# Optimization experiments

Measured on AMD Instinct MI355X. Metric: run time of the kernel, lower is better.

The kernel has to match this reference:

```python
import jax, jax.numpy as jnp
from jax import lax
import numpy as np

COST_CLASS, COST_BOX, COST_GIOU = 1.0, 5.0, 2.0
B, Q, C, T = 16, 900, 92, 100
INF = jnp.float32(1e18)


def setup_inputs() -> dict:
    key = jax.random.key(0)
    k1, k2, k3, k4 = jax.random.split(key, 4)
    pred_logits = jax.random.normal(k1, (B, Q, C), jnp.float32)

    def mk_boxes(k, n):
        kc, ks = jax.random.split(k)
        cxcy = jax.random.uniform(kc, (B, n, 2), jnp.float32) * 0.8 + 0.1
        wh = jax.random.uniform(ks, (B, n, 2), jnp.float32) * 0.2 + 0.05
        return jnp.concatenate([cxcy, wh], axis=-1)  # valid cxcywh in (0,1)

    pred_boxes = mk_boxes(k2, Q)
    tgt_boxes = mk_boxes(k3, T)
    tgt_labels = jax.random.randint(k4, (B, T), 0, C)
    return {"pred_logits": pred_logits, "pred_boxes": pred_boxes,
            "tgt_labels": tgt_labels, "tgt_boxes": tgt_boxes}


def box_cxcywh_to_xyxy(b):
    cx, cy, w, h = b[..., 0], b[..., 1], b[..., 2], b[..., 3]
    return jnp.stack([cx - 0.5 * w, cy - 0.5 * h, cx + 0.5 * w, cy + 0.5 * h], axis=-1)


def generalized_box_iou(a, b):
    # a: [B,Q,4] xyxy, b: [B,T,4] xyxy -> [B,Q,T]
    area_a = (a[..., 2] - a[..., 0]) * (a[..., 3] - a[..., 1])  # [B,Q]
    area_b = (b[..., 2] - b[..., 0]) * (b[..., 3] - b[..., 1])  # [B,T]
    a_ = a[:, :, None, :]
    b_ = b[:, None, :, :]
    lt = jnp.maximum(a_[..., :2], b_[..., :2])
    rb = jnp.minimum(a_[..., 2:], b_[..., 2:])
    wh = jnp.clip(rb - lt, 0.0)
    inter = wh[..., 0] * wh[..., 1]
    union = area_a[:, :, None] + area_b[:, None, :] - inter
    iou = inter / union
    lt_c = jnp.minimum(a_[..., :2], b_[..., :2])
    rb_c = jnp.maximum(a_[..., 2:], b_[..., 2:])
    wh_c = jnp.clip(rb_c - lt_c, 0.0)
    area_c = wh_c[..., 0] * wh_c[..., 1]
    return iou - (area_c - union) / area_c


def cost_matrix(pred_logits, pred_boxes, tgt_labels, tgt_boxes):
    probs = jax.nn.softmax(pred_logits, axis=-1)                         # [B,Q,C]
    cost_class = -jnp.take_along_axis(probs, tgt_labels[:, None, :], 2)  # [B,Q,T]
    cost_box = jnp.abs(pred_boxes[:, :, None, :] - tgt_boxes[:, None, :, :]).sum(-1)
    cost_giou = -generalized_box_iou(box_cxcywh_to_xyxy(pred_boxes),
                                     box_cxcywh_to_xyxy(tgt_boxes))
    return COST_BOX * cost_box + COST_CLASS * cost_class + COST_GIOU * cost_giou


def hungarian(cost):
    # Jonker-Volgenant shortest augmenting path. cost: [n, m], n <= m, minimize.
    # Returns col_for_row [n]: column assigned to each row.
    n, m = cost.shape

    def solve_row(i, uvp):
        u, v, p = uvp  # u:[n+1] row potentials, v:[m+1] col potentials, p:[m+1] col->row (n = free)
        p = p.at[m].set(i)  # virtual start column holds current row
        minv = jnp.full((m,), INF, jnp.float32)
        way = jnp.zeros((m,), jnp.int32)
        used = jnp.zeros((m + 1,), bool)
        j0 = jnp.int32(m)

        def cond(s):
            _, _, _, _, _, j0 = s
            return p[j0] != n  # stop when a free column is reached

        def body(s):
            u, v, minv, way, used, j0 = s
            used = used.at[j0].set(True)
            i0 = p[j0]
            cur = cost[i0] - u[i0] - v[:m]           # reduced costs of row i0
            mask = (~used[:m]) & (cur < minv)
            minv = jnp.where(mask, cur, minv)
            way = jnp.where(mask, j0, way)
            mvals = jnp.where(used[:m], INF, minv)
            j1 = jnp.argmin(mvals).astype(jnp.int32)
            delta = mvals[j1]
            u = u.at[p].add(jnp.where(used, delta, 0.0))
            v = v - jnp.where(used, delta, 0.0)
            minv = jnp.where(used[:m], minv, minv - delta)
            return (u, v, minv, way, used, j1)

        u, v, minv, way, used, j0 = lax.while_loop(cond, body, (u, v, minv, way, used, j0))

        def acond(s):
            _, j0 = s
            return j0 != m

        def abody(s):
            p, j0 = s
            j1 = way[j0]
            p = p.at[j0].set(p[j1])
            return (p, j1)

        p, _ = lax.while_loop(acond, abody, (p, j0))
        return (u, v, p)

    u0 = jnp.zeros((n + 1,), jnp.float32)
    v0 = jnp.zeros((m + 1,), jnp.float32)
    p0 = jnp.full((m + 1,), n, jnp.int32)
    _, _, p = lax.fori_loop(0, n, solve_row, (u0, v0, p0))
    col_for_row = jnp.zeros((n + 1,), jnp.int32).at[p[:m]].set(
        jnp.arange(m, dtype=jnp.int32))[:n]
    return col_for_row


def reference(pred_logits, pred_boxes, tgt_labels, tgt_boxes):
    cost = cost_matrix(pred_logits, pred_boxes, tgt_labels, tgt_boxes)  # [B,Q,T]
    # assign each target (row) to a distinct query (col); vmap over batch
    q_per_t = jax.vmap(hungarian)(jnp.swapaxes(cost, 1, 2))  # [B,T]
    order = jnp.argsort(q_per_t, axis=-1)                    # sort by query idx (scipy convention)
    q_idx = jnp.take_along_axis(q_per_t, order, axis=-1)     # query indices  [B,T]
    t_idx = order.astype(jnp.int32)                          # target indices [B,T]
    return cost, q_idx, t_idx
```

## Files before the change

kernel.cpp:

```cpp
#include <hip/hip_runtime.h>

#define BB 16
#define QQ 900
#define QP 960
#define VIRT QP
#define CC 92
#define TT 100
#define INFF 1e18f
#define NK 15

#define DPP_STEP_F(x, ctrl, OP)                                             \
  do {                                                                      \
    float _o = __int_as_float(__builtin_amdgcn_update_dpp(                  \
        __float_as_int(x), __float_as_int(x), (ctrl), 0xF, 0xF, false));    \
    (x) = OP((x), _o);                                                      \
  } while (0)

__device__ __forceinline__ float wave_fmax63(float x) {
  DPP_STEP_F(x, 0xB1, fmaxf);
  DPP_STEP_F(x, 0x4E, fmaxf);
  DPP_STEP_F(x, 0x141, fmaxf);
  DPP_STEP_F(x, 0x140, fmaxf);
  DPP_STEP_F(x, 0x142, fmaxf);
  DPP_STEP_F(x, 0x143, fmaxf);
  return x;
}
__device__ __forceinline__ float wave_fmin63(float x) {
  DPP_STEP_F(x, 0xB1, fminf);
  DPP_STEP_F(x, 0x4E, fminf);
  DPP_STEP_F(x, 0x141, fminf);
  DPP_STEP_F(x, 0x140, fminf);
  DPP_STEP_F(x, 0x142, fminf);
  DPP_STEP_F(x, 0x143, fminf);
  return x;
}
__device__ __forceinline__ float wave_fadd63(float x) {
#define ADDF(a, b) ((a) + (b))
  DPP_STEP_F(x, 0xB1, ADDF);
  DPP_STEP_F(x, 0x4E, ADDF);
  DPP_STEP_F(x, 0x141, ADDF);
  DPP_STEP_F(x, 0x140, ADDF);
  DPP_STEP_F(x, 0x142, ADDF);
  DPP_STEP_F(x, 0x143, ADDF);
#undef ADDF
  return x;
}
__device__ __forceinline__ int wave_imin63(int x) {
  {int _o=__builtin_amdgcn_update_dpp(x,x,0xB1,0xF,0xF,false); x=_o<x?_o:x;}
  {int _o=__builtin_amdgcn_update_dpp(x,x,0x4E,0xF,0xF,false); x=_o<x?_o:x;}
  {int _o=__builtin_amdgcn_update_dpp(x,x,0x141,0xF,0xF,false);x=_o<x?_o:x;}
  {int _o=__builtin_amdgcn_update_dpp(x,x,0x140,0xF,0xF,false);x=_o<x?_o:x;}
  {int _o=__builtin_amdgcn_update_dpp(x,x,0x142,0xF,0xF,false);x=_o<x?_o:x;}
  {int _o=__builtin_amdgcn_update_dpp(x,x,0x143,0xF,0xF,false);x=_o<x?_o:x;}
  return x;
}

#define KEY_STEP(CTRL)                                                      \
  do {                                                                      \
    unsigned olo = (unsigned)__builtin_amdgcn_update_dpp(                   \
        (int)klo, (int)klo, (CTRL), 0xF, 0xF, false);                       \
    unsigned ohi = (unsigned)__builtin_amdgcn_update_dpp(                   \
        (int)khi, (int)khi, (CTRL), 0xF, 0xF, false);                       \
    const unsigned long long cur8 =                                         \
        ((unsigned long long)khi << 32) | klo;                              \
    const unsigned long long oth8 =                                         \
        ((unsigned long long)ohi << 32) | olo;                              \
    if (oth8 < cur8) { khi = ohi; klo = olo; }                              \
  } while (0)

__device__ __forceinline__ void stage_row(const float* __restrict__ row,
                                          float* buf, int lane) {
  typedef __attribute__((address_space(1))) const void gv_t;
  typedef __attribute__((address_space(3))) void lv_t;
  __builtin_amdgcn_global_load_lds((gv_t*)(row + lane * 4),       (lv_t*)(buf),       16, 0, 0);
  __builtin_amdgcn_global_load_lds((gv_t*)(row + 256 + lane * 4), (lv_t*)(buf + 256), 16, 0, 0);
  __builtin_amdgcn_global_load_lds((gv_t*)(row + 512 + lane * 4), (lv_t*)(buf + 512), 16, 0, 0);
  __builtin_amdgcn_global_load_lds((gv_t*)(row + 768 + lane),     (lv_t*)(buf + 768), 4, 0, 0);
  __builtin_amdgcn_global_load_lds((gv_t*)(row + 832 + lane),     (lv_t*)(buf + 832), 4, 0, 0);
  __builtin_amdgcn_global_load_lds((gv_t*)(row + 896 + lane),     (lv_t*)(buf + 896), 4, 0, 0);
}

__device__ __forceinline__ int p_get(unsigned a, unsigned b, unsigned c,
                                     unsigned d, int j) {
  const int l = j & 63, kq = j >> 6;
  unsigned r0 = (unsigned)__builtin_amdgcn_readlane((int)a, l);
  unsigned r1 = (unsigned)__builtin_amdgcn_readlane((int)b, l);
  unsigned r2 = (unsigned)__builtin_amdgcn_readlane((int)c, l);
  unsigned r3 = (unsigned)__builtin_amdgcn_readlane((int)d, l);
  unsigned r = (kq < 8) ? (kq < 4 ? r0 : r1) : (kq < 12 ? r2 : r3);
  return (int)((r >> ((kq & 3) * 8)) & 0xFFu);
}

#define P_SET(jj, val)                                                      \
  do {                                                                      \
    const int _j = (jj); const int _kq = _j >> 6;                           \
    const unsigned _sh = (unsigned)((_kq & 3) * 8);                         \
    const unsigned _nm = ~(0xFFu << _sh);                                   \
    const unsigned _in = ((unsigned)(val) & 0xFFu) << _sh;                  \
    const bool _own = (lane == (_j & 63));                                  \
    if (_kq < 4)       { if (_own) p4a = (p4a & _nm) | _in; }               \
    else if (_kq < 8)  { if (_own) p4b = (p4b & _nm) | _in; }               \
    else if (_kq < 12) { if (_own) p4c = (p4c & _nm) | _in; }               \
    else               { if (_own) p4d = (p4d & _nm) | _in; }               \
  } while (0)

__global__ __launch_bounds__(64) void cost_kernel(
    const float* __restrict__ logits,
    const float* __restrict__ pboxes,
    const int*   __restrict__ tlabels,
    const float* __restrict__ tboxes,
    float* __restrict__ cost,
    float* __restrict__ costT,
    int ctp)
{
  const int bq   = blockIdx.x;
  const int b    = bq / QQ;
  const int q    = bq - b * QQ;
  const int lane = threadIdx.x;

  __shared__ float sl[CC];

  const float a = logits[(size_t)bq * CC + lane];
  const float bb2 = (lane < CC - 64)
                        ? logits[(size_t)bq * CC + 64 + lane]
                        : -3.402823466e38f;

  float mx = fmaxf(a, bb2);
  mx = wave_fmax63(mx);
  const float m = __int_as_float(
      __builtin_amdgcn_readlane(__float_as_int(mx), 63));

  const float e0 = expf(a - m);
  const float e1 = (lane < CC - 64) ? expf(bb2 - m) : 0.0f;
  sl[lane] = e0;
  if (lane < CC - 64) sl[64 + lane] = e1;

  float sm = e0 + e1;
  sm = wave_fadd63(sm);
  const float ssum = __int_as_float(
      __builtin_amdgcn_readlane(__float_as_int(sm), 63));

  const float4 pbv = ((const float4*)pboxes)[bq];
  const float pax1 = pbv.x - 0.5f * pbv.z, pay1 = pbv.y - 0.5f * pbv.w;
  const float pax2 = pbv.x + 0.5f * pbv.z, pay2 = pbv.y + 0.5f * pbv.w;
  const float area_a = (pax2 - pax1) * (pay2 - pay1);

  for (int t = lane; t < TT; t += 64) {
    const int lab = tlabels[b * TT + t];
    const float cc = -(sl[lab] / ssum);

    const float4 tb = ((const float4*)tboxes)[b * TT + t];
    const float cbox = fabsf(pbv.x - tb.x) + fabsf(pbv.y - tb.y) +
                       fabsf(pbv.z - tb.z) + fabsf(pbv.w - tb.w);

    const float bx1 = tb.x - 0.5f * tb.z, by1 = tb.y - 0.5f * tb.w;
    const float bx2 = tb.x + 0.5f * tb.z, by2 = tb.y + 0.5f * tb.w;
    const float area_b = (bx2 - bx1) * (by2 - by1);

    const float ltx = fmaxf(pax1, bx1), lty = fmaxf(pay1, by1);
    const float rbx = fminf(pax2, bx2), rby = fminf(pay2, by2);
    const float iw = fmaxf(rbx - ltx, 0.0f), ih = fmaxf(rby - lty, 0.0f);
    const float inter = iw * ih;
    const float uni = area_a + area_b - inter;
    const float iou = inter / uni;

    const float cx1 = fminf(pax1, bx1), cy1 = fminf(pay1, by1);
    const float cx2 = fmaxf(pax2, bx2), cy2 = fmaxf(pay2, by2);
    const float cw = fmaxf(cx2 - cx1, 0.0f), ch = fmaxf(cy2 - cy1, 0.0f);
    const float ac = cw * ch;
    const float giou = iou - (ac - uni) / ac;

    const float cval = 5.0f * cbox + cc - 2.0f * giou;
    cost[(size_t)bq * TT + t] = cval;
    if (ctp) costT[((size_t)b * TT + t) * ctp + q] = cval;
  }
  if (ctp == QP && q < QP - QQ) {
    for (int t = lane; t < TT; t += 64)
      costT[((size_t)b * TT + t) * QP + QQ + q] = INFF;
  }
}

__global__ void __launch_bounds__(64)
hungarianT_kernel(
    const float* __restrict__ ct,
    float* __restrict__ out_q,
    float* __restrict__ out_t)
{
  const int b    = blockIdx.x;
  const int lane = threadIdx.x;

  __shared__ __align__(16) float rowbuf[2][QP];
  __shared__ int way_lds[QP];
  __shared__ int qpt[TT];

  const float* __restrict__ base = ct + (size_t)b * TT * QP;

  unsigned p4a = 0x64646464u, p4b = 0x64646464u;
  unsigned p4c = 0x64646464u, p4d = 0x64646464u;

  float u0 = 0.0f, u1 = 0.0f;
  float v[NK];
#pragma unroll
  for (int k = 0; k < NK; ++k) v[k] = 0.0f;

  stage_row(base, &rowbuf[0][0], lane);

  for (int i = 0; i < TT; ++i) {
    float* bufc = &rowbuf[i & 1][0];
    float* bufn = &rowbuf[(i + 1) & 1][0];

    float minv[NK];
#pragma unroll
    for (int k = 0; k < NK; ++k) minv[k] = INFF;
    unsigned umask = 0;

    int i0 = i;
    int j0 = VIRT;
    int jfin;

    float us = (i0 < 64) ? u0 : u1;
    float ui0 = __int_as_float(
        __builtin_amdgcn_readlane(__float_as_int(us), i0 & 63));

    for (int step = 0; step < 128; ++step) {
      if (i0 == lane)      umask |= (1u << 30);
      if (i0 == 64 + lane) umask |= (1u << 31);
      if (j0 != VIRT && (j0 & 63) == lane) umask |= (1u << (j0 >> 6));

      asm volatile("s_waitcnt vmcnt(0)" ::: "memory");

      float lmin  = INFF;
      int   kbest = 0;
#pragma unroll
      for (int k = 0; k < NK; ++k) {
        const float ck  = bufc[k * 64 + lane];
        const bool  uk  = (umask >> k) & 1u;
        const float cur = ck - ui0 - v[k];
        const bool  imp = !uk && (cur < minv[k]);
        if (imp) { minv[k] = cur; way_lds[k * 64 + lane] = j0; }
        const float eff = uk ? INFF : minv[k];
        if (eff < lmin) { lmin = eff; kbest = k; }
      }
      const int lidx = (kbest << 6) + lane;

      if (j0 == VIRT && i + 1 < TT)
        stage_row(base + (size_t)(i + 1) * QP, bufn, lane);

      unsigned fb = __float_as_uint(lmin);
      fb = (fb & 0x80000000u) ? ~fb : (fb | 0x80000000u);
      unsigned khi = fb, klo = (unsigned)lidx;
      KEY_STEP(0xB1);
      KEY_STEP(0x4E);
      KEY_STEP(0x141);
      KEY_STEP(0x140);
      KEY_STEP(0x142);
      KEY_STEP(0x143);
      const int j1 = __builtin_amdgcn_readlane((int)klo, 63);
      const unsigned hb =
          (unsigned)__builtin_amdgcn_readlane((int)khi, 63);
      const float delta =
          __uint_as_float((hb & 0x80000000u) ? (hb ^ 0x80000000u) : ~hb);

      const int  i0n = p_get(p4a, p4b, p4c, p4d, j1);
      const bool fin = (i0n == TT);

      if (!fin) stage_row(base + (size_t)i0n * QP, bufc, lane);

      u0 += ((umask >> 30) & 1u) ? delta : 0.0f;
      u1 += (umask >> 31)        ? delta : 0.0f;
#pragma unroll
      for (int k = 0; k < NK; ++k)
        v[k] -= ((umask >> k) & 1u) ? delta : 0.0f;
      if (!fin) {
#pragma unroll
        for (int k = 0; k < NK; ++k)
          minv[k] -= ((umask >> k) & 1u) ? 0.0f : delta;
      }

      if (fin) { jfin = j1; break; }
      float us2 = (i0n < 64) ? u0 : u1;
      ui0 = __int_as_float(
          __builtin_amdgcn_readlane(__float_as_int(us2), i0n & 63));
      j0 = j1;
      i0 = i0n;
    }

    if (j0 == VIRT) {
      P_SET(jfin, i);
    } else {
      int j = jfin;
      for (int hop = 0; hop < 128 && j != VIRT; ++hop) {
        int jn = way_lds[j];
        jn = __builtin_amdgcn_readfirstlane(jn);
        const int pj = (jn == VIRT) ? i : p_get(p4a, p4b, p4c, p4d, jn);
        P_SET(j, pj);
        j = jn;
      }
    }
  }

#pragma unroll
  for (int k = 0; k < NK; ++k) {
    const unsigned reg = (k < 4) ? p4a : (k < 8) ? p4b : (k < 12) ? p4c : p4d;
    const int r = (int)((reg >> ((k & 3) * 8)) & 0xFFu);
    const int j = k * 64 + lane;
    if (r < TT) qpt[r] = j;
  }
  __syncthreads();

  for (int t = lane; t < TT; t += 64) {
    const int myq = qpt[t];
    int rank = 0;
    for (int t2 = 0; t2 < TT; ++t2) rank += (qpt[t2] < myq) ? 1 : 0;
    out_q[b * TT + rank] = (float)myq;
    out_t[b * TT + rank] = (float)t;
  }
}

__global__ void __launch_bounds__(64)
hungarian_kernel(
    const float* __restrict__ cost,
    const float* __restrict__ costT,
    float* __restrict__ out_q,
    float* __restrict__ out_t)
{
  const int b    = blockIdx.x;
  const int lane = threadIdx.x;

  __shared__ int p_lds[QQ + 1];
  __shared__ int way_lds[QQ];
  __shared__ int qpt[TT];

  const float* base;
  size_t rs, cs;
  if (costT) { base = costT + (size_t)b * TT * QQ; rs = QQ; cs = 1; }
  else       { base = cost  + (size_t)b * QQ * TT; rs = 1;  cs = TT; }

  for (int j = lane; j <= QQ; j += 64) p_lds[j] = TT;

  float u0 = 0.0f, u1 = 0.0f;
  float v[NK];
#pragma unroll
  for (int k = 0; k < NK; ++k) v[k] = 0.0f;

  float c[NK];
#pragma unroll
  for (int k = 0; k < NK; ++k) {
    const int j = k * 64 + lane;
    c[k] = (j < QQ) ? base[(size_t)j * cs] : 0.0f;
  }

  for (int i = 0; i < TT; ++i) {
    p_lds[QQ] = i;

    float minv[NK];
#pragma unroll
    for (int k = 0; k < NK; ++k) minv[k] = INFF;
    unsigned umask = 0;
    bool t0 = false, t1 = false;

    int i0 = i;
    int j0 = QQ;
    int jfin;

    float us = (i0 < 64) ? u0 : u1;
    float ui0 = __int_as_float(
        __builtin_amdgcn_readlane(__float_as_int(us), i0 & 63));

    while (true) {
      t0 = t0 || (i0 == lane);
      t1 = t1 || (i0 == 64 + lane);
      if (j0 != QQ) {
        if ((j0 & 63) == lane) umask |= (1u << (j0 >> 6));
      }

      float lmin = INFF;
      int   lidx = QQ;
#pragma unroll
      for (int k = 0; k < NK; ++k) {
        const int j = k * 64 + lane;
        if (j < QQ && !((umask >> k) & 1u)) {
          const float cur = c[k] - ui0 - v[k];
          if (cur < minv[k]) { minv[k] = cur; way_lds[j] = j0; }
          if (minv[k] < lmin) { lmin = minv[k]; lidx = j; }
        }
      }

      float red = wave_fmin63(lmin);
      const float delta = __int_as_float(
          __builtin_amdgcn_readlane(__float_as_int(red), 63));
      int cand = (lmin == delta) ? lidx : 0x7FFFFFFF;
      int redi = wave_imin63(cand);
      const int j1 = __builtin_amdgcn_readlane(redi, 63);

      int i0n = p_lds[j1];
      i0n = __builtin_amdgcn_readfirstlane(i0n);
      const bool fin = (i0n == TT);

      u0 += t0 ? delta : 0.0f;
      u1 += t1 ? delta : 0.0f;
#pragma unroll
      for (int k = 0; k < NK; ++k) {
        const bool uk = (umask >> k) & 1u;
        v[k]    -= uk ? delta : 0.0f;
        minv[k] -= uk ? 0.0f  : delta;
      }

      if (!fin) {
        float us2 = (i0n < 64) ? u0 : u1;
        ui0 = __int_as_float(
            __builtin_amdgcn_readlane(__float_as_int(us2), i0n & 63));
#pragma unroll
        for (int k = 0; k < NK; ++k) {
          const int j = k * 64 + lane;
          if (j < QQ) c[k] = base[(size_t)i0n * rs + (size_t)j * cs];
        }
      }
      asm volatile("" ::: "memory");

      if (fin) { jfin = j1; break; }
      j0 = j1;
      i0 = i0n;
    }

    if (i + 1 < TT) {
#pragma unroll
      for (int k = 0; k < NK; ++k) {
        const int jj = k * 64 + lane;
        if (jj < QQ) c[k] = base[(size_t)(i + 1) * rs + (size_t)jj * cs];
      }
    }

    int j = jfin;
    while (j != QQ) {
      const int jn = way_lds[j];
      const int pj = p_lds[jn];
      p_lds[j] = pj;
      j = jn;
    }
    asm volatile("" ::: "memory");
  }

#pragma unroll
  for (int k = 0; k < NK; ++k) {
    const int j = k * 64 + lane;
    if (j < QQ) {
      const int r = p_lds[j];
      if (r < TT) qpt[r] = j;
    }
  }
  __syncthreads();

  for (int t = lane; t < TT; t += 64) {
    const int myq = qpt[t];
    int rank = 0;
    for (int t2 = 0; t2 < TT; ++t2) rank += (qpt[t2] < myq) ? 1 : 0;
    out_q[b * TT + rank] = (float)myq;
    out_t[b * TT + rank] = (float)t;
  }
}

extern "C" void kernel_launch(void* const* d_in, const int* in_sizes, int n_in,
                              void* d_out, int out_size, void* d_ws, size_t ws_size,
                              hipStream_t stream) {
  const float* logits  = (const float*)d_in[0];
  const float* pboxes  = (const float*)d_in[1];
  const int*   tlabels = (const int*)d_in[2];
  const float* tboxes  = (const float*)d_in[3];

  float* out  = (float*)d_out;
  float* cost = out;
  float* oq   = out + (size_t)BB * QQ * TT;
  float* ot   = oq + (size_t)BB * TT;

  const size_t padded_bytes = (size_t)BB * TT * QP * sizeof(float);
  const size_t plain_bytes  = (size_t)BB * TT * QQ * sizeof(float);

  if (ws_size >= padded_bytes) {
    float* costT = (float*)d_ws;
    hipLaunchKernelGGL(cost_kernel, dim3(BB * QQ), dim3(64), 0, stream,
                       logits, pboxes, tlabels, tboxes, cost, costT, QP);
    hipLaunchKernelGGL(hungarianT_kernel, dim3(BB), dim3(64), 0, stream,
                       costT, oq, ot);
  } else if (ws_size >= plain_bytes) {
    float* costT = (float*)d_ws;
    hipLaunchKernelGGL(cost_kernel, dim3(BB * QQ), dim3(64), 0, stream,
                       logits, pboxes, tlabels, tboxes, cost, costT, QQ);
    hipLaunchKernelGGL(hungarian_kernel, dim3(BB), dim3(64), 0, stream,
                       cost, costT, oq, ot);
  } else {
    hipLaunchKernelGGL(cost_kernel, dim3(BB * QQ), dim3(64), 0, stream,
                       logits, pboxes, tlabels, tboxes, cost, (float*)nullptr, 0);
    hipLaunchKernelGGL(hungarian_kernel, dim3(BB), dim3(64), 0, stream,
                       cost, (const float*)nullptr, oq, ot);
  }
}
```

Before: 219.3 us.

## Load Hungarian cost rows into registers and stamp way entries to skip writes

The shortest-augmenting-path loop now keeps the current cost row in registers. Inside the inner loop, rows are loaded directly from global memory into those registers instead of being staged through a double-buffered LDS row, which drops the per-step LDS reads and the second buffer. Only the first row of each target is prefetched through a single LDS buffer. Way entries are tagged with the row index as a stamp, so the writes for the virtual column can be skipped, and stale entries read during the backtrack count as the virtual column. The risk is that global-load latency now falls directly on the dependent inner loop without the LDS staging, and register pressure goes up.

```diff
diff --git a/kernel.cpp b/kernel.cpp
--- a/kernel.cpp
+++ b/kernel.cpp
@@ -189,12 +189,15 @@
   const int b    = blockIdx.x;
   const int lane = threadIdx.x;
 
-  __shared__ __align__(16) float rowbuf[2][QP];
+  __shared__ __align__(16) float rowbuf[QP];
   __shared__ int way_lds[QP];
   __shared__ int qpt[TT];
 
   const float* __restrict__ base = ct + (size_t)b * TT * QP;
 
+#pragma unroll
+  for (int k = 0; k < NK; ++k) way_lds[k * 64 + lane] = -1;
+
   unsigned p4a = 0x64646464u, p4b = 0x64646464u;
   unsigned p4c = 0x64646464u, p4d = 0x64646464u;
 
@@ -203,16 +206,21 @@
 #pragma unroll
   for (int k = 0; k < NK; ++k) v[k] = 0.0f;
 
-  stage_row(base, &rowbuf[0][0], lane);
+  stage_row(base, &rowbuf[0], lane);
 
   for (int i = 0; i < TT; ++i) {
-    float* bufc = &rowbuf[i & 1][0];
-    float* bufn = &rowbuf[(i + 1) & 1][0];
+    asm volatile("s_waitcnt vmcnt(0)" ::: "memory");
+    float c[NK];
+#pragma unroll
+    for (int k = 0; k < NK; ++k) c[k] = rowbuf[k * 64 + lane];
+    asm volatile("s_waitcnt lgkmcnt(0)" ::: "memory");
+    if (i + 1 < TT) stage_row(base + (size_t)(i + 1) * QP, &rowbuf[0], lane);
 
     float minv[NK];
 #pragma unroll
     for (int k = 0; k < NK; ++k) minv[k] = INFF;
     unsigned umask = 0;
+    const int stamp = i << 12;
 
     int i0 = i;
     int j0 = VIRT;
@@ -227,24 +235,23 @@
       if (i0 == 64 + lane) umask |= (1u << 31);
       if (j0 != VIRT && (j0 & 63) == lane) umask |= (1u << (j0 >> 6));
 
-      asm volatile("s_waitcnt vmcnt(0)" ::: "memory");
+      const bool dowrite = (j0 != VIRT);
 
       float lmin  = INFF;
       int   kbest = 0;
 #pragma unroll
       for (int k = 0; k < NK; ++k) {
-        const float ck  = bufc[k * 64 + lane];
         const bool  uk  = (umask >> k) & 1u;
-        const float cur = ck - ui0 - v[k];
+        const float cur = c[k] - ui0 - v[k];
         const bool  imp = !uk && (cur < minv[k]);
-        if (imp) { minv[k] = cur; way_lds[k * 64 + lane] = j0; }
+        if (imp) {
+          minv[k] = cur;
+          if (dowrite) way_lds[k * 64 + lane] = stamp | j0;
+        }
         const float eff = uk ? INFF : minv[k];
         if (eff < lmin) { lmin = eff; kbest = k; }
       }
       const int lidx = (kbest << 6) + lane;
-
-      if (j0 == VIRT && i + 1 < TT)
-        stage_row(base + (size_t)(i + 1) * QP, bufn, lane);
 
       unsigned fb = __float_as_uint(lmin);
       fb = (fb & 0x80000000u) ? ~fb : (fb | 0x80000000u);
@@ -264,7 +271,11 @@
       const int  i0n = p_get(p4a, p4b, p4c, p4d, j1);
       const bool fin = (i0n == TT);
 
-      if (!fin) stage_row(base + (size_t)i0n * QP, bufc, lane);
+      if (!fin) {
+        const float* __restrict__ prow = base + (size_t)i0n * QP;
+#pragma unroll
+        for (int k = 0; k < NK; ++k) c[k] = prow[k * 64 + lane];
+      }
 
       u0 += ((umask >> 30) & 1u) ? delta : 0.0f;
       u1 += (umask >> 31)        ? delta : 0.0f;
@@ -290,8 +301,9 @@
     } else {
       int j = jfin;
       for (int hop = 0; hop < 128 && j != VIRT; ++hop) {
-        int jn = way_lds[j];
-        jn = __builtin_amdgcn_readfirstlane(jn);
+        int raw = way_lds[j];
+        raw = __builtin_amdgcn_readfirstlane(raw);
+        const int jn = ((raw >> 12) == i) ? (raw & 0xFFF) : VIRT;
         const int pj = (jn == VIRT) ? i : p_get(p4a, p4b, p4c, p4d, jn);
         P_SET(j, pj);
         j = jn;
```

After: 215.9 us. About the same (-1.5%).
